# Optimization experiments

Measured on AMD Instinct MI355X. Metric: run time of the kernel, lower is better.

## Reference

```python
import jax, jax.numpy as jnp
import numpy as np

N = 50000       # nodes
E = 800000      # directed edges (before self-loops)
D_IN = 128
H = 32          # hidden width, heads=1 (PyG SuperGATConv defaults)
D_OUT = 16
L = 15          # stacked SuperGATConv layers
NEG_SLOPE = 0.2


def setup_inputs() -> dict:
    key = jax.random.key(0)
    ks = jax.random.split(key, 8)
    s_in = 1.0 / np.sqrt(D_IN)
    s_h = 1.0 / np.sqrt(H)
    return dict(
        x=jax.random.normal(ks[0], (N, D_IN), jnp.float32),
        edge_index=jax.random.randint(ks[1], (2, E), 0, N, jnp.int32),
        W0=jax.random.normal(ks[2], (D_IN, H), jnp.float32) * s_in,
        b0=jnp.zeros((H,), jnp.float32),
        Ws=jax.random.normal(ks[3], (L, H, H), jnp.float32) * s_h,
        att_l=jax.random.normal(ks[4], (L, H), jnp.float32) * s_h,
        att_r=jax.random.normal(ks[5], (L, H), jnp.float32) * s_h,
        bs=jnp.zeros((L, H), jnp.float32),
        W16=jax.random.normal(ks[6], (H, D_OUT), jnp.float32) * s_h,
        b16=jnp.zeros((D_OUT,), jnp.float32),
    )


def _supergat(h, src, dst, W, al, ar, b):
    # One SuperGATConv (attention_type='MX', heads=1, concat) forward.
    hp = h @ W                          # [N, H] transformed features
    hj = hp[src]                        # [E', H] source (message) features
    hi = hp[dst]                        # [E', H] destination features
    logits = jnp.sum(hi * hj, axis=-1)  # MX dot-product logits
    alpha = hj @ al + hi @ ar           # GAT-style additive scores
    alpha = alpha * jax.nn.sigmoid(logits)
    alpha = jnp.where(alpha >= 0, alpha, NEG_SLOPE * alpha)  # leaky_relu
    # segment softmax over destination nodes
    amax = jax.ops.segment_max(alpha, dst, num_segments=N)
    ex = jnp.exp(alpha - amax[dst])
    den = jax.ops.segment_sum(ex, dst, num_segments=N)
    coef = ex / den[dst]
    out = jax.ops.segment_sum(hj * coef[:, None], dst, num_segments=N)
    return out + b


def reference(x, edge_index, W0, b0, Ws, att_l, att_r, bs, W16, b16):
    # PyG SuperGATConv adds self-loops by default
    loops = jnp.arange(N, dtype=edge_index.dtype)
    src = jnp.concatenate([edge_index[0], loops])
    dst = jnp.concatenate([edge_index[1], loops])
    h = x @ W0 + b0                     # conv0: Linear(in, 32)

    def step(h, p):
        W, al, ar, b = p
        return jax.nn.relu(_supergat(h, src, dst, W, al, ar, b)), None

    h, _ = jax.lax.scan(step, h, (Ws, att_l, att_r, bs))
    return h @ W16 + b16                # conv16: Linear(32, out)
```

## Files before the change

kernel.cpp:

```cpp
#include <hip/hip_runtime.h>
#include <hip/hip_fp16.h>
#include <cmath>
#include <cstring>

#define NN 50000
#define EE 800000
#define ET 850000
#define PADCAP 1004544
#define NBK 831
#define EBINS 196
#define DB 512
#define NB 50

__global__ void k_fill(int* __restrict__ p){
  int i = blockIdx.x*256 + threadIdx.x;
  p[i] = NN;
}

__global__ void k_permfill(int* __restrict__ perm){
  int i = blockIdx.x*256 + threadIdx.x;
  perm[i] = NN;
}

__global__ __launch_bounds__(1024) void k_ebhist(const int* __restrict__ ei,
                                                 int* __restrict__ ebh){
  __shared__ int hist[EBINS];
  int t = threadIdx.x, b = blockIdx.x;
  if (t < EBINS) hist[t] = 0;
  __syncthreads();
  int e = b*1024 + t;
  if (e < ET){
    int d = (e < EE) ? ei[EE + e] : (e - EE);
    atomicAdd(&hist[d >> 8], 1);
  }
  __syncthreads();
  if (t < EBINS) ebh[t*NBK + b] = hist[t];
}

__global__ __launch_bounds__(1024) void k_escan1(const int* __restrict__ ebh,
                                                 int* __restrict__ ebhoff,
                                                 int* __restrict__ btot){
  __shared__ int tmp[1024];
  int bin = blockIdx.x, t = threadIdx.x;
  int v = (t < NBK) ? ebh[bin*NBK + t] : 0;
  int inc = v;
  for (int off = 1; off < 1024; off <<= 1){
    tmp[t] = inc; __syncthreads();
    int add = (t >= off) ? tmp[t - off] : 0;
    __syncthreads();
    inc += add;
  }
  if (t < NBK) ebhoff[bin*NBK + t] = inc - v;
  if (t == 1023) btot[bin] = inc;
}

__global__ __launch_bounds__(256) void k_escan2(const int* __restrict__ btot,
                                                int* __restrict__ bbase){
  __shared__ int tmp[256];
  int t = threadIdx.x;
  int v = (t < EBINS) ? btot[t] : 0;
  int inc = v;
  for (int off = 1; off < 256; off <<= 1){
    tmp[t] = inc; __syncthreads();
    int add = (t >= off) ? tmp[t - off] : 0;
    __syncthreads();
    inc += add;
  }
  if (t < EBINS) bbase[t] = inc - v;
  if (t == 255) bbase[EBINS] = inc;
}

__global__ __launch_bounds__(1024) void k_ebin(const int* __restrict__ ei,
                                               const int* __restrict__ ebhoff,
                                               const int* __restrict__ bbase,
                                               int2* __restrict__ ebuf){
  __shared__ int hist[EBINS];
  int t = threadIdx.x, b = blockIdx.x;
  if (t < EBINS) hist[t] = 0;
  __syncthreads();
  int e = b*1024 + t;
  if (e < ET){
    int s, d;
    if (e < EE){ s = ei[e]; d = ei[EE + e]; } else { s = d = e - EE; }
    int bin = d >> 8;
    int rank = atomicAdd(&hist[bin], 1);
    int pos = bbase[bin] + ebhoff[bin*NBK + b] + rank;
    ebuf[pos] = make_int2(s, d);
  }
}

__global__ __launch_bounds__(1024) void k_ecnt(const int2* __restrict__ ebuf,
                                               const int* __restrict__ bbase,
                                               int* __restrict__ count){
  __shared__ int cnt[256];
  int t = threadIdx.x, bin = blockIdx.x;
  if (t < 256) cnt[t] = 0;
  __syncthreads();
  int rb = bbase[bin], re = bbase[bin+1];
  for (int i = rb + t; i < re; i += 1024) atomicAdd(&cnt[ebuf[i].y - (bin << 8)], 1);
  __syncthreads();
  int idx = (bin << 8) + t;
  if (t < 256 && idx < NN) count[idx] = cnt[t];
}

__global__ void k_bsum(const int* __restrict__ count, int* __restrict__ bsums){
  int i = blockIdx.x*256 + threadIdx.x;
  int v = (i < NN) ? ((count[i] + 3) & ~3) : 0;
  #pragma unroll
  for (int m = 1; m < 64; m <<= 1) v += __shfl_xor(v, m);
  __shared__ int ws[4];
  if ((threadIdx.x & 63) == 0) ws[threadIdx.x >> 6] = v;
  __syncthreads();
  if (threadIdx.x == 0) bsums[blockIdx.x] = ws[0] + ws[1] + ws[2] + ws[3];
}

__global__ void k_bscan(const int* __restrict__ bsums, int* __restrict__ boffs, int nb){
  __shared__ int tmp[256];
  int t = threadIdx.x;
  int self = (t < nb) ? bsums[t] : 0;
  int v = self;
  for (int off = 1; off < 256; off <<= 1){
    tmp[t] = v; __syncthreads();
    int add = (t >= off) ? tmp[t - off] : 0;
    __syncthreads();
    v += add;
  }
  if (t < nb) boffs[t] = v - self;
}

__global__ void k_scan(const int* __restrict__ count, const int* __restrict__ boffs,
                       int* __restrict__ offs){
  __shared__ int tmp[256];
  int t = threadIdx.x;
  int gid = blockIdx.x*256 + t;
  int self = (gid < NN) ? ((count[gid] + 3) & ~3) : 0;
  int v = self;
  for (int off = 1; off < 256; off <<= 1){
    tmp[t] = v; __syncthreads();
    int add = (t >= off) ? tmp[t - off] : 0;
    __syncthreads();
    v += add;
  }
  int excl = v - self + boffs[blockIdx.x];
  if (gid < NN) offs[gid] = excl;
  if (gid == NN-1) offs[NN] = excl + self;
}

__global__ __launch_bounds__(1024) void k_escatter(const int2* __restrict__ ebuf,
                                                   const int* __restrict__ bbase,
                                                   const int* __restrict__ offs,
                                                   int* __restrict__ srcCSR){
  __shared__ int cur[256];
  int t = threadIdx.x, bin = blockIdx.x;
  if (t < 256){ int idx = (bin << 8) + t; cur[t] = (idx < NN) ? offs[idx] : 0; }
  __syncthreads();
  int rb = bbase[bin], re = bbase[bin+1];
  for (int i = rb + t; i < re; i += 1024){
    int2 e = ebuf[i];
    int p = atomicAdd(&cur[e.y - (bin << 8)], 1);
    srcCSR[p] = e.x;
  }
}

__global__ __launch_bounds__(1024) void k_dhist_blk(const int* __restrict__ count,
                                                    int* __restrict__ blockhist){
  __shared__ int hist[DB];
  int t = threadIdx.x, b = blockIdx.x;
  if (t < DB) hist[t] = 0;
  __syncthreads();
  int i = b*1024 + t;
  if (i < NN){
    int deg = count[i]; if (deg > DB-1) deg = DB-1;
    atomicAdd(&hist[DB-1-deg], 1);
  }
  __syncthreads();
  if (t < DB) blockhist[t*NB + b] = hist[t];
}

__global__ __launch_bounds__(DB) void k_dcol(const int* __restrict__ blockhist,
                                             int* __restrict__ blockoffs,
                                             int* __restrict__ dbase){
  int k = threadIdx.x;
  int run = 0;
  #pragma unroll 5
  for (int b = 0; b < NB; ++b){
    int v = blockhist[k*NB + b];
    blockoffs[k*NB + b] = run;
    run += v;
  }
  __shared__ int tmp[DB];
  int v = run;
  for (int off = 1; off < DB; off <<= 1){
    tmp[k] = v; __syncthreads();
    int add = (k >= off) ? tmp[k - off] : 0;
    __syncthreads();
    v += add;
  }
  dbase[k] = v - run;
}

__global__ __launch_bounds__(1024) void k_dscatter_blk(const int* __restrict__ count,
                                                       const int* __restrict__ blockoffs,
                                                       const int* __restrict__ dbase,
                                                       int* __restrict__ perm){
  __shared__ int hist[DB];
  int t = threadIdx.x, b = blockIdx.x;
  if (t < DB) hist[t] = 0;
  __syncthreads();
  int i = b*1024 + t;
  if (i < NN){
    int deg = count[i]; if (deg > DB-1) deg = DB-1;
    int bin = DB-1-deg;
    int rank = atomicAdd(&hist[bin], 1);
    int pos = dbase[bin] + blockoffs[bin*NB + b] + rank;
    perm[pos] = i;
  }
}

__device__ __forceinline__ float4 cvt_row(uint2 r){
  __half2 h0, h1;
  memcpy(&h0, &r.x, 4); memcpy(&h1, &r.y, 4);
  float2 f0 = __half22float2(h0), f1 = __half22float2(h1);
  return make_float4(f0.x, f0.y, f1.x, f1.y);
}
__device__ __forceinline__ unsigned pack_h2(float x, float y){
  __half2 h = __floats2half2_rn(x, y);
  unsigned u; memcpy(&u, &h, 4); return u;
}

__global__ __launch_bounds__(256) void k_prologue(
    const float* __restrict__ x, const float* __restrict__ W0, const float* __restrict__ b0,
    const float* __restrict__ Ws0, const float* __restrict__ al0, const float* __restrict__ ar0,
    __half* __restrict__ hp_out, float* __restrict__ hl_out, float* __restrict__ hr_out){
  __shared__ __align__(16) float w0[128*32];
  __shared__ __align__(16) float w1[32*32];
  int t = threadIdx.x;
  for (int i = t; i < 4096; i += 256) w0[i] = W0[i];
  for (int i = t; i < 1024; i += 256) w1[i] = Ws0[i];
  __syncthreads();
  int g = t >> 5, lane = t & 31;
  int n = blockIdx.x*8 + g;
  const float4* x4 = (const float4*)(x + (size_t)n*128);
  float h = b0[lane];
  #pragma unroll
  for (int j4 = 0; j4 < 32; ++j4){
    float4 xv = x4[j4];
    h += xv.x * w0[(j4*4+0)*32 + lane];
    h += xv.y * w0[(j4*4+1)*32 + lane];
    h += xv.z * w0[(j4*4+2)*32 + lane];
    h += xv.w * w0[(j4*4+3)*32 + lane];
  }
  float hp = 0.f;
  #pragma unroll
  for (int j = 0; j < 32; ++j) hp += __shfl(h, j, 32) * w1[j*32 + lane];
  float tl = hp*al0[lane], tr = hp*ar0[lane];
  #pragma unroll
  for (int m = 1; m < 32; m <<= 1){ tl += __shfl_xor(tl, m); tr += __shfl_xor(tr, m); }
  hp_out[(size_t)n*32 + lane] = __float2half(hp);
  if (lane == 0){ hl_out[n] = tl; hr_out[n] = tr; }
  if (blockIdx.x == 0){
    if (g == 0) hp_out[(size_t)NN*32 + lane] = __float2half(0.f);
    if (t == 0) hl_out[NN] = -1e30f;
  }
}

__global__ __launch_bounds__(256) void k_layer(
    const __half* __restrict__ hp, const float* __restrict__ hl, const float* __restrict__ hr,
    const int* __restrict__ offs, const int* __restrict__ srcCSR, const int* __restrict__ perm,
    const float* __restrict__ bcur,
    const float* __restrict__ Wn, const float* __restrict__ aln, const float* __restrict__ arn,
    const float* __restrict__ b16,
    __half* __restrict__ hp_out, float* __restrict__ hl_out, float* __restrict__ hr_out,
    float* __restrict__ final_out, int last){
  __shared__ __align__(16) float wl[1024];
  __shared__ __align__(16) float xb[32*36];
  int t = threadIdx.x;
  int nW = last ? 512 : 1024;
  for (int i = t; i < nW; i += 256) wl[i] = Wn[i];
  __syncthreads();
  int lane = t & 63;
  int li = lane & 7;
  int slot = t >> 3;
  int d = perm[blockIdx.x*32 + slot];
  int beg = offs[d];
  int lenP = offs[d+1] - beg;
  int ng = (d < NN) ? (lenP >> 2) : 0;
  float4 hpd4 = cvt_row(*(const uint2*)(hp + ((size_t)d << 5) + (li << 2)));
  float hrd = hr[d];

  int maxg = ng;
  #pragma unroll
  for (int m = 1; m < 64; m <<= 1) maxg = max(maxg, __shfl_xor(maxg, m));

  auto LD4 = [&](int g)->int4{
    int4 q = *(const int4*)(srcCSR + beg + (g << 2));
    if (g >= ng){ q.x = NN; q.y = NN; q.z = NN; q.w = NN; }
    return q;
  };
  auto ROW = [&](int s)->uint2{
    return *(const uint2*)(hp + ((size_t)s << 5) + (li << 2));
  };
  float4 acc = {0.f,0.f,0.f,0.f};
  float den = 0.f;
  auto EDGE = [&](uint2 r, float g){
    float4 v = cvt_row(r);
    float p = v.x*hpd4.x + v.y*hpd4.y + v.z*hpd4.z + v.w*hpd4.w;
    p += __shfl_xor(p, 1); p += __shfl_xor(p, 2); p += __shfl_xor(p, 4);
    float a = (g + hrd) * (1.f/(1.f + __expf(-p)));
    a = fmaxf(a, 0.2f*a);
    float e = __expf(a);
    den += e;
    acc.x += v.x*e; acc.y += v.y*e; acc.z += v.z*e; acc.w += v.w*e;
  };

  int4 qA = LD4(0);
  uint2 rA0=ROW(qA.x), rA1=ROW(qA.y), rA2=ROW(qA.z), rA3=ROW(qA.w);
  float gA0=hl[qA.x], gA1=hl[qA.y], gA2=hl[qA.z], gA3=hl[qA.w];
  int4 qB = LD4(1);

  for (int g = 0; g < maxg; g += 2){
    uint2 rB0=ROW(qB.x), rB1=ROW(qB.y), rB2=ROW(qB.z), rB3=ROW(qB.w);
    float gB0=hl[qB.x], gB1=hl[qB.y], gB2=hl[qB.z], gB3=hl[qB.w];
    int4 qN = LD4(g + 2);
    EDGE(rA0,gA0); EDGE(rA1,gA1); EDGE(rA2,gA2); EDGE(rA3,gA3);
    rA0=ROW(qN.x); rA1=ROW(qN.y); rA2=ROW(qN.z); rA3=ROW(qN.w);
    gA0=hl[qN.x]; gA1=hl[qN.y]; gA2=hl[qN.z]; gA3=hl[qN.w];
    qB = LD4(g + 3);
    EDGE(rB0,gB0); EDGE(rB1,gB1); EDGE(rB2,gB2); EDGE(rB3,gB3);
  }

  float rden = 1.f/den;
  float4 b4 = *((const float4*)bcur + li);
  float4 h4;
  h4.x = fmaxf(acc.x*rden + b4.x, 0.f);
  h4.y = fmaxf(acc.y*rden + b4.y, 0.f);
  h4.z = fmaxf(acc.z*rden + b4.z, 0.f);
  h4.w = fmaxf(acc.w*rden + b4.w, 0.f);
  float* hrow = xb + slot*36;
  *((float4*)hrow + li) = h4;

  if (!last){
    float4 o = {0.f,0.f,0.f,0.f};
    #pragma unroll
    for (int q = 0; q < 8; ++q){
      float4 hq = *((const float4*)hrow + q);
      float4 w0 = *(const float4*)(wl + (4*q+0)*32 + 4*li);
      float4 w1 = *(const float4*)(wl + (4*q+1)*32 + 4*li);
      float4 w2 = *(const float4*)(wl + (4*q+2)*32 + 4*li);
      float4 w3 = *(const float4*)(wl + (4*q+3)*32 + 4*li);
      o.x += hq.x*w0.x + hq.y*w1.x + hq.z*w2.x + hq.w*w3.x;
      o.y += hq.x*w0.y + hq.y*w1.y + hq.z*w2.y + hq.w*w3.y;
      o.z += hq.x*w0.z + hq.y*w1.z + hq.z*w2.z + hq.w*w3.z;
      o.w += hq.x*w0.w + hq.y*w1.w + hq.z*w2.w + hq.w*w3.w;
    }
    float4 a4 = *((const float4*)aln + li);
    float4 r4 = *((const float4*)arn + li);
    float tl = o.x*a4.x + o.y*a4.y + o.z*a4.z + o.w*a4.w;
    float tr = o.x*r4.x + o.y*r4.y + o.z*r4.z + o.w*r4.w;
    tl += __shfl_xor(tl, 1); tl += __shfl_xor(tl, 2); tl += __shfl_xor(tl, 4);
    tr += __shfl_xor(tr, 1); tr += __shfl_xor(tr, 2); tr += __shfl_xor(tr, 4);
    if (d < NN){
      uint2 st; st.x = pack_h2(o.x, o.y); st.y = pack_h2(o.z, o.w);
      *(uint2*)(hp_out + ((size_t)d << 5) + (li << 2)) = st;
      if (li == 0){ hl_out[d] = tl; hr_out[d] = tr; }
    }
    if (blockIdx.x == 0){
      if (t < 32) hp_out[(size_t)NN*32 + t] = __float2half(0.f);
      if (t == 0) hl_out[NN] = -1e30f;
    }
  } else {
    const float2* b2p = (const float2*)b16;
    float2 o = b2p[li];
    #pragma unroll
    for (int q = 0; q < 8; ++q){
      float4 hq = *((const float4*)hrow + q);
      float2 w0 = *(const float2*)(wl + (4*q+0)*16 + 2*li);
      float2 w1 = *(const float2*)(wl + (4*q+1)*16 + 2*li);
      float2 w2 = *(const float2*)(wl + (4*q+2)*16 + 2*li);
      float2 w3 = *(const float2*)(wl + (4*q+3)*16 + 2*li);
      o.x += hq.x*w0.x + hq.y*w1.x + hq.z*w2.x + hq.w*w3.x;
      o.y += hq.x*w0.y + hq.y*w1.y + hq.z*w2.y + hq.w*w3.y;
    }
    if (d < NN) *((float2*)(final_out + (size_t)d*16) + li) = o;
  }
}

extern "C" void kernel_launch(void* const* d_in, const int* in_sizes, int n_in,
                              void* d_out, int out_size, void* d_ws, size_t ws_size,
                              hipStream_t stream){
  const float* x   = (const float*)d_in[0];
  const int*   ei  = (const int*)  d_in[1];
  const float* W0  = (const float*)d_in[2];
  const float* b0  = (const float*)d_in[3];
  const float* Ws  = (const float*)d_in[4];
  const float* al  = (const float*)d_in[5];
  const float* ar  = (const float*)d_in[6];
  const float* bs  = (const float*)d_in[7];
  const float* W16 = (const float*)d_in[8];
  const float* b16 = (const float*)d_in[9];
  float* out = (float*)d_out;

  char* w = (char*)d_ws;
  int* count     = (int*)w;   w += 50176*sizeof(int);
  int* offs      = (int*)w;   w += 50432*sizeof(int);
  int* srcCSR    = (int*)w;   w += (size_t)PADCAP*sizeof(int);
  int* bsums     = (int*)w;   w += 256*sizeof(int);
  int* boffs     = (int*)w;   w += 256*sizeof(int);
  int* perm      = (int*)w;   w += 50176*sizeof(int);
  int* blockhist = (int*)w;   w += DB*NB*sizeof(int);
  int* blockoffs = (int*)w;   w += DB*NB*sizeof(int);
  int* dbase     = (int*)w;   w += DB*sizeof(int);
  int* ebh       = (int*)w;   w += (size_t)EBINS*NBK*sizeof(int) + 16;
  int* ebhoff    = (int*)w;   w += (size_t)EBINS*NBK*sizeof(int) + 16;
  int* btot      = (int*)w;   w += 256*sizeof(int);
  int* bbase     = (int*)w;   w += 256*sizeof(int);
  int2* ebuf     = (int2*)w;  w += (size_t)(NBK*1024)*sizeof(int2);
  __half* hpA  = (__half*)w; w += (size_t)(NN+16)*32*sizeof(__half);
  __half* hpB  = (__half*)w; w += (size_t)(NN+16)*32*sizeof(__half);
  float* hlA   = (float*)w; w += 50176*sizeof(float);
  float* hrA   = (float*)w; w += 50176*sizeof(float);
  float* hlB   = (float*)w; w += 50176*sizeof(float);
  float* hrB   = (float*)w; w += 50176*sizeof(float);

  k_fill    <<<PADCAP/256, 256, 0, stream>>>(srcCSR);
  k_permfill<<<196, 256, 0, stream>>>(perm);
  k_ebhist  <<<NBK, 1024, 0, stream>>>(ei, ebh);
  k_escan1  <<<EBINS, 1024, 0, stream>>>(ebh, ebhoff, btot);
  k_escan2  <<<1, 256, 0, stream>>>(btot, bbase);
  k_ebin    <<<NBK, 1024, 0, stream>>>(ei, ebhoff, bbase, ebuf);
  k_ecnt    <<<EBINS, 1024, 0, stream>>>(ebuf, bbase, count);
  k_bsum    <<<196, 256, 0, stream>>>(count, bsums);
  k_bscan   <<<1, 256, 0, stream>>>(bsums, boffs, 196);
  k_scan    <<<196, 256, 0, stream>>>(count, boffs, offs);
  k_escatter<<<EBINS, 1024, 0, stream>>>(ebuf, bbase, offs, srcCSR);
  k_dhist_blk   <<<NB, 1024, 0, stream>>>(count, blockhist);
  k_dcol        <<<1,  DB,   0, stream>>>(blockhist, blockoffs, dbase);
  k_dscatter_blk<<<NB, 1024, 0, stream>>>(count, blockoffs, dbase, perm);

  k_prologue<<<6250, 256, 0, stream>>>(x, W0, b0, Ws, al, ar, hpA, hlA, hrA);

  int nblk = (NN + 31) / 32 + 1;
  for (int l = 0; l < 15; ++l){
    const __half* hin = (l & 1) ? hpB : hpA;
    const float* hlin = (l & 1) ? hlB : hlA;
    const float* hrin = (l & 1) ? hrB : hrA;
    __half* hout = (l & 1) ? hpA : hpB;
    float* hlout = (l & 1) ? hlA : hlB;
    float* hrout = (l & 1) ? hrA : hrB;
    int last = (l == 14);
    const float* Wn  = last ? W16 : (Ws + (size_t)(l+1)*1024);
    const float* aln = last ? al  : (al + (size_t)(l+1)*32);
    const float* arn = last ? ar  : (ar + (size_t)(l+1)*32);
    k_layer<<<nblk, 256, 0, stream>>>(hin, hlin, hrin, offs, srcCSR, perm,
                                      bs + (size_t)l*32,
                                      Wn, aln, arn, b16,
                                      hout, hlout, hrout, out, last);
  }
}
```

Baseline: 496.7 us.

## Gather 16-byte rows with four lanes per node and batch prologue rows

The layer kernel now assigns 4 lanes per destination node instead of 8. Each lane loads 8 half features as one 16-byte load, so a block covers 64 nodes, the dot-product reduction needs fewer shuffles, and the next-layer matvec is restructured to match. The __syncthreads for the shared weights moves after the gather loop, so the weight load overlaps with edge processing. The prologue handles 32 nodes per block, two interleaved rows per warp for more instruction-level parallelism, with clamped indices for the tail. The cost is more registers per thread for the wider prefetched rows and accumulators, which could lower occupancy.

```diff
diff --git a/kernel.cpp b/kernel.cpp
--- a/kernel.cpp
+++ b/kernel.cpp
@@ -217,11 +217,12 @@
   }
 }
 
-__device__ __forceinline__ float4 cvt_row(uint2 r){
-  __half2 h0, h1;
-  memcpy(&h0, &r.x, 4); memcpy(&h1, &r.y, 4);
-  float2 f0 = __half22float2(h0), f1 = __half22float2(h1);
-  return make_float4(f0.x, f0.y, f1.x, f1.y);
+__device__ __forceinline__ void cvt8(uint4 r, float* v){
+  __half2 h;
+  memcpy(&h, &r.x, 4); float2 f = __half22float2(h); v[0]=f.x; v[1]=f.y;
+  memcpy(&h, &r.y, 4); f = __half22float2(h); v[2]=f.x; v[3]=f.y;
+  memcpy(&h, &r.z, 4); f = __half22float2(h); v[4]=f.x; v[5]=f.y;
+  memcpy(&h, &r.w, 4); f = __half22float2(h); v[6]=f.x; v[7]=f.y;
 }
 __device__ __forceinline__ unsigned pack_h2(float x, float y){
   __half2 h = __floats2half2_rn(x, y);
@@ -239,27 +240,48 @@
   for (int i = t; i < 1024; i += 256) w1[i] = Ws0[i];
   __syncthreads();
   int g = t >> 5, lane = t & 31;
-  int n = blockIdx.x*8 + g;
-  const float4* x4 = (const float4*)(x + (size_t)n*128);
-  float h = b0[lane];
+  float bl = b0[lane], alv = al0[lane], arv = ar0[lane];
   #pragma unroll
-  for (int j4 = 0; j4 < 32; ++j4){
-    float4 xv = x4[j4];
-    h += xv.x * w0[(j4*4+0)*32 + lane];
-    h += xv.y * w0[(j4*4+1)*32 + lane];
-    h += xv.z * w0[(j4*4+2)*32 + lane];
-    h += xv.w * w0[(j4*4+3)*32 + lane];
-  }
-  float hp = 0.f;
-  #pragma unroll
-  for (int j = 0; j < 32; ++j) hp += __shfl(h, j, 32) * w1[j*32 + lane];
-  float tl = hp*al0[lane], tr = hp*ar0[lane];
-  #pragma unroll
-  for (int m = 1; m < 32; m <<= 1){ tl += __shfl_xor(tl, m); tr += __shfl_xor(tr, m); }
-  hp_out[(size_t)n*32 + lane] = __float2half(hp);
-  if (lane == 0){ hl_out[n] = tl; hr_out[n] = tr; }
+  for (int p = 0; p < 2; ++p){
+    int na = blockIdx.x*32 + p*16 + g;
+    int nb = na + 8;
+    int nac = (na < NN) ? na : NN-1;
+    int nbc = (nb < NN) ? nb : NN-1;
+    const float4* xa = (const float4*)(x + (size_t)nac*128);
+    const float4* xb4 = (const float4*)(x + (size_t)nbc*128);
+    float ha = bl, hb = bl;
+    #pragma unroll
+    for (int j4 = 0; j4 < 32; ++j4){
+      float4 va = xa[j4], vb = xb4[j4];
+      float c0 = w0[(j4*4+0)*32 + lane], c1 = w0[(j4*4+1)*32 + lane];
+      float c2 = w0[(j4*4+2)*32 + lane], c3 = w0[(j4*4+3)*32 + lane];
+      ha += va.x*c0 + va.y*c1 + va.z*c2 + va.w*c3;
+      hb += vb.x*c0 + vb.y*c1 + vb.z*c2 + vb.w*c3;
+    }
+    float hpa = 0.f, hpb = 0.f;
+    #pragma unroll
+    for (int j = 0; j < 32; ++j){
+      float w = w1[j*32 + lane];
+      hpa += __shfl(ha, j, 32) * w;
+      hpb += __shfl(hb, j, 32) * w;
+    }
+    float tla = hpa*alv, tra = hpa*arv, tlb = hpb*alv, trb = hpb*arv;
+    #pragma unroll
+    for (int m = 1; m < 32; m <<= 1){
+      tla += __shfl_xor(tla, m); tra += __shfl_xor(tra, m);
+      tlb += __shfl_xor(tlb, m); trb += __shfl_xor(trb, m);
+    }
+    if (na < NN){
+      hp_out[(size_t)na*32 + lane] = __float2half(hpa);
+      if (lane == 0){ hl_out[na] = tla; hr_out[na] = tra; }
+    }
+    if (nb < NN){
+      hp_out[(size_t)nb*32 + lane] = __float2half(hpb);
+      if (lane == 0){ hl_out[nb] = tlb; hr_out[nb] = trb; }
+    }
+  }
   if (blockIdx.x == 0){
-    if (g == 0) hp_out[(size_t)NN*32 + lane] = __float2half(0.f);
+    if (t < 32) hp_out[(size_t)NN*32 + t] = __float2half(0.f);
     if (t == 0) hl_out[NN] = -1e30f;
   }
 }
@@ -273,19 +295,19 @@
     __half* __restrict__ hp_out, float* __restrict__ hl_out, float* __restrict__ hr_out,
     float* __restrict__ final_out, int last){
   __shared__ __align__(16) float wl[1024];
-  __shared__ __align__(16) float xb[32*36];
+  __shared__ __align__(16) float xb[64*36];
   int t = threadIdx.x;
   int nW = last ? 512 : 1024;
   for (int i = t; i < nW; i += 256) wl[i] = Wn[i];
-  __syncthreads();
   int lane = t & 63;
-  int li = lane & 7;
-  int slot = t >> 3;
-  int d = perm[blockIdx.x*32 + slot];
+  int li = lane & 3;
+  int slot = t >> 2;
+  int d = perm[blockIdx.x*64 + slot];
   int beg = offs[d];
   int lenP = offs[d+1] - beg;
   int ng = (d < NN) ? (lenP >> 2) : 0;
-  float4 hpd4 = cvt_row(*(const uint2*)(hp + ((size_t)d << 5) + (li << 2)));
+  float hpd[8];
+  cvt8(*(const uint4*)(hp + ((size_t)d << 5) + (li << 3)), hpd);
   float hrd = hr[d];
 
   int maxg = ng;
@@ -297,29 +319,32 @@
     if (g >= ng){ q.x = NN; q.y = NN; q.z = NN; q.w = NN; }
     return q;
   };
-  auto ROW = [&](int s)->uint2{
-    return *(const uint2*)(hp + ((size_t)s << 5) + (li << 2));
+  auto ROW = [&](int s)->uint4{
+    return *(const uint4*)(hp + ((size_t)s << 5) + (li << 3));
   };
-  float4 acc = {0.f,0.f,0.f,0.f};
+  float acc[8] = {0.f,0.f,0.f,0.f,0.f,0.f,0.f,0.f};
   float den = 0.f;
-  auto EDGE = [&](uint2 r, float g){
-    float4 v = cvt_row(r);
-    float p = v.x*hpd4.x + v.y*hpd4.y + v.z*hpd4.z + v.w*hpd4.w;
-    p += __shfl_xor(p, 1); p += __shfl_xor(p, 2); p += __shfl_xor(p, 4);
-    float a = (g + hrd) * (1.f/(1.f + __expf(-p)));
+  auto EDGE = [&](uint4 r, float gl){
+    float v[8];
+    cvt8(r, v);
+    float p = v[0]*hpd[0] + v[1]*hpd[1] + v[2]*hpd[2] + v[3]*hpd[3]
+            + v[4]*hpd[4] + v[5]*hpd[5] + v[6]*hpd[6] + v[7]*hpd[7];
+    p += __shfl_xor(p, 1); p += __shfl_xor(p, 2);
+    float a = (gl + hrd) * (1.f/(1.f + __expf(-p)));
     a = fmaxf(a, 0.2f*a);
     float e = __expf(a);
     den += e;
-    acc.x += v.x*e; acc.y += v.y*e; acc.z += v.z*e; acc.w += v.w*e;
+    #pragma unroll
+    for (int k = 0; k < 8; ++k) acc[k] += v[k]*e;
   };
 
   int4 qA = LD4(0);
-  uint2 rA0=ROW(qA.x), rA1=ROW(qA.y), rA2=ROW(qA.z), rA3=ROW(qA.w);
+  uint4 rA0=ROW(qA.x), rA1=ROW(qA.y), rA2=ROW(qA.z), rA3=ROW(qA.w);
   float gA0=hl[qA.x], gA1=hl[qA.y], gA2=hl[qA.z], gA3=hl[qA.w];
   int4 qB = LD4(1);
 
   for (int g = 0; g < maxg; g += 2){
-    uint2 rB0=ROW(qB.x), rB1=ROW(qB.y), rB2=ROW(qB.z), rB3=ROW(qB.w);
+    uint4 rB0=ROW(qB.x), rB1=ROW(qB.y), rB2=ROW(qB.z), rB3=ROW(qB.w);
     float gB0=hl[qB.x], gB1=hl[qB.y], gB2=hl[qB.z], gB3=hl[qB.w];
     int4 qN = LD4(g + 2);
     EDGE(rA0,gA0); EDGE(rA1,gA1); EDGE(rA2,gA2); EDGE(rA3,gA3);
@@ -330,38 +355,50 @@
   }
 
   float rden = 1.f/den;
-  float4 b4 = *((const float4*)bcur + li);
-  float4 h4;
-  h4.x = fmaxf(acc.x*rden + b4.x, 0.f);
-  h4.y = fmaxf(acc.y*rden + b4.y, 0.f);
-  h4.z = fmaxf(acc.z*rden + b4.z, 0.f);
-  h4.w = fmaxf(acc.w*rden + b4.w, 0.f);
+  const float4* bc4 = (const float4*)bcur;
+  float4 ba = bc4[2*li], bb = bc4[2*li+1];
   float* hrow = xb + slot*36;
-  *((float4*)hrow + li) = h4;
-
+  {
+    float4 h0, h1;
+    h0.x = fmaxf(acc[0]*rden + ba.x, 0.f);
+    h0.y = fmaxf(acc[1]*rden + ba.y, 0.f);
+    h0.z = fmaxf(acc[2]*rden + ba.z, 0.f);
+    h0.w = fmaxf(acc[3]*rden + ba.w, 0.f);
+    h1.x = fmaxf(acc[4]*rden + bb.x, 0.f);
+    h1.y = fmaxf(acc[5]*rden + bb.y, 0.f);
+    h1.z = fmaxf(acc[6]*rden + bb.z, 0.f);
+    h1.w = fmaxf(acc[7]*rden + bb.w, 0.f);
+    *((float4*)hrow + 2*li) = h0;
+    *((float4*)hrow + 2*li + 1) = h1;
+  }
+  __syncthreads();
+
+  const float4* wl4 = (const float4*)wl;
   if (!last){
-    float4 o = {0.f,0.f,0.f,0.f};
-    #pragma unroll
-    for (int q = 0; q < 8; ++q){
-      float4 hq = *((const float4*)hrow + q);
-      float4 w0 = *(const float4*)(wl + (4*q+0)*32 + 4*li);
-      float4 w1 = *(const float4*)(wl + (4*q+1)*32 + 4*li);
-      float4 w2 = *(const float4*)(wl + (4*q+2)*32 + 4*li);
-      float4 w3 = *(const float4*)(wl + (4*q+3)*32 + 4*li);
-      o.x += hq.x*w0.x + hq.y*w1.x + hq.z*w2.x + hq.w*w3.x;
-      o.y += hq.x*w0.y + hq.y*w1.y + hq.z*w2.y + hq.w*w3.y;
-      o.z += hq.x*w0.z + hq.y*w1.z + hq.z*w2.z + hq.w*w3.z;
-      o.w += hq.x*w0.w + hq.y*w1.w + hq.z*w2.w + hq.w*w3.w;
-    }
-    float4 a4 = *((const float4*)aln + li);
-    float4 r4 = *((const float4*)arn + li);
-    float tl = o.x*a4.x + o.y*a4.y + o.z*a4.z + o.w*a4.w;
-    float tr = o.x*r4.x + o.y*r4.y + o.z*r4.z + o.w*r4.w;
-    tl += __shfl_xor(tl, 1); tl += __shfl_xor(tl, 2); tl += __shfl_xor(tl, 4);
-    tr += __shfl_xor(tr, 1); tr += __shfl_xor(tr, 2); tr += __shfl_xor(tr, 4);
+    float o[8] = {0.f,0.f,0.f,0.f,0.f,0.f,0.f,0.f};
+    #pragma unroll
+    for (int k = 0; k < 32; ++k){
+      float hk = hrow[k];
+      float4 wa = wl4[k*8 + 2*li];
+      float4 wb = wl4[k*8 + 2*li + 1];
+      o[0]+=hk*wa.x; o[1]+=hk*wa.y; o[2]+=hk*wa.z; o[3]+=hk*wa.w;
+      o[4]+=hk*wb.x; o[5]+=hk*wb.y; o[6]+=hk*wb.z; o[7]+=hk*wb.w;
+    }
+    const float4* a4 = (const float4*)aln;
+    const float4* r4 = (const float4*)arn;
+    float4 aa = a4[2*li], ab = a4[2*li+1];
+    float4 ra = r4[2*li], rb = r4[2*li+1];
+    float tl = o[0]*aa.x+o[1]*aa.y+o[2]*aa.z+o[3]*aa.w
+             + o[4]*ab.x+o[5]*ab.y+o[6]*ab.z+o[7]*ab.w;
+    float tr = o[0]*ra.x+o[1]*ra.y+o[2]*ra.z+o[3]*ra.w
+             + o[4]*rb.x+o[5]*rb.y+o[6]*rb.z+o[7]*rb.w;
+    tl += __shfl_xor(tl, 1); tl += __shfl_xor(tl, 2);
+    tr += __shfl_xor(tr, 1); tr += __shfl_xor(tr, 2);
     if (d < NN){
-      uint2 st; st.x = pack_h2(o.x, o.y); st.y = pack_h2(o.z, o.w);
-      *(uint2*)(hp_out + ((size_t)d << 5) + (li << 2)) = st;
+      uint4 st;
+      st.x = pack_h2(o[0], o[1]); st.y = pack_h2(o[2], o[3]);
+      st.z = pack_h2(o[4], o[5]); st.w = pack_h2(o[6], o[7]);
+      *(uint4*)(hp_out + ((size_t)d << 5) + (li << 3)) = st;
       if (li == 0){ hl_out[d] = tl; hr_out[d] = tr; }
     }
     if (blockIdx.x == 0){
@@ -369,19 +406,14 @@
       if (t == 0) hl_out[NN] = -1e30f;
     }
   } else {
-    const float2* b2p = (const float2*)b16;
-    float2 o = b2p[li];
-    #pragma unroll
-    for (int q = 0; q < 8; ++q){
-      float4 hq = *((const float4*)hrow + q);
-      float2 w0 = *(const float2*)(wl + (4*q+0)*16 + 2*li);
-      float2 w1 = *(const float2*)(wl + (4*q+1)*16 + 2*li);
-      float2 w2 = *(const float2*)(wl + (4*q+2)*16 + 2*li);
-      float2 w3 = *(const float2*)(wl + (4*q+3)*16 + 2*li);
-      o.x += hq.x*w0.x + hq.y*w1.x + hq.z*w2.x + hq.w*w3.x;
-      o.y += hq.x*w0.y + hq.y*w1.y + hq.z*w2.y + hq.w*w3.y;
-    }
-    if (d < NN) *((float2*)(final_out + (size_t)d*16) + li) = o;
+    float4 o = ((const float4*)b16)[li];
+    #pragma unroll
+    for (int k = 0; k < 32; ++k){
+      float hk = hrow[k];
+      float4 wv = wl4[k*4 + li];
+      o.x += hk*wv.x; o.y += hk*wv.y; o.z += hk*wv.z; o.w += hk*wv.w;
+    }
+    if (d < NN) *((float4*)(final_out + (size_t)d*16) + li) = o;
   }
 }
 
@@ -437,9 +469,9 @@
   k_dcol        <<<1,  DB,   0, stream>>>(blockhist, blockoffs, dbase);
   k_dscatter_blk<<<NB, 1024, 0, stream>>>(count, blockoffs, dbase, perm);
 
-  k_prologue<<<6250, 256, 0, stream>>>(x, W0, b0, Ws, al, ar, hpA, hlA, hrA);
-
-  int nblk = (NN + 31) / 32 + 1;
+  k_prologue<<<1563, 256, 0, stream>>>(x, W0, b0, Ws, al, ar, hpA, hlA, hrA);
+
+  int nblk = (50048) / 64;
   for (int l = 0; l < 15; ++l){
     const __half* hin = (l & 1) ? hpB : hpA;
     const float* hlin = (l & 1) ? hlB : hlA;
```

After: 497.4 us. No clear change (+0.1%).
